# Performance work log

Measured on AMD Instinct MI355X. Metric: run time of the kernel, lower is better.

## Reference

```python
import jax, jax.numpy as jnp
import numpy as np

B, T, IN, H, OUT = 256, 512, 9, 512, 3


def setup_inputs() -> dict:
    key = jax.random.key(0)
    ks = jax.random.split(key, 7)
    s = 0.05  # keep gates in a sane range
    return {
        "x": jax.random.normal(ks[0], (B, T, IN), dtype=jnp.float32),
        "W_ih": jax.random.normal(ks[1], (4 * H, IN), dtype=jnp.float32) * s,
        "W_hh": jax.random.normal(ks[2], (4 * H, H), dtype=jnp.float32) * s,
        "b_ih": jax.random.normal(ks[3], (4 * H,), dtype=jnp.float32) * s,
        "b_hh": jax.random.normal(ks[4], (4 * H,), dtype=jnp.float32) * s,
        "W_fc": jax.random.normal(ks[5], (OUT, H), dtype=jnp.float32) * s,
        "b_fc": jax.random.normal(ks[6], (OUT,), dtype=jnp.float32) * s,
        "horizon": 10,
    }


def reference(x, W_ih, W_hh, b_ih, b_hh, W_fc, b_fc, horizon):
    Bn, Tn, _ = x.shape
    Hn = W_hh.shape[1]
    On = W_fc.shape[0]
    # branch condition depends only on the static step index -> precompute mask
    idx = np.arange(Tn)
    use_raw = jnp.asarray((idx < 5) | (idx % int(horizon) == 0))  # [T]

    def step(carry, inp):
        hx, cx, prev_out = carry
        x_t, raw = inp  # x_t: [B, IN], raw: scalar bool
        # else-branch input: previous fc output (3) ++ last 6 state features -> 9
        alt = jnp.concatenate([prev_out, x_t[:, On:]], axis=1)
        xin = jnp.where(raw, x_t, alt)
        gates = xin @ W_ih.T + b_ih + hx @ W_hh.T + b_hh  # [B, 4H]
        i, f, g, o = jnp.split(gates, 4, axis=1)
        cx2 = jax.nn.sigmoid(f) * cx + jax.nn.sigmoid(i) * jnp.tanh(g)
        hx2 = jax.nn.sigmoid(o) * jnp.tanh(cx2)
        out = hx2 @ W_fc.T + b_fc  # [B, OUT]
        return (hx2, cx2, out), out

    init = (
        jnp.zeros((Bn, Hn), x.dtype),
        jnp.zeros((Bn, Hn), x.dtype),
        jnp.zeros((Bn, On), x.dtype),
    )
    x_tb = jnp.swapaxes(x, 0, 1)  # [T, B, IN]
    _, outs = jax.lax.scan(step, init, (x_tb, use_raw))
    return jnp.swapaxes(outs, 0, 1)  # [B, T, OUT]
```

## Files before the change

kernel.cpp:

```cpp
#include <hip/hip_runtime.h>

typedef __attribute__((ext_vector_type(8))) short bf16x8;
typedef __attribute__((ext_vector_type(4))) float f32x4;

#define NTT 512
#define NH  512
#define NIN 9
#define NO  3
#define MEMBERS 32
#define MROWS   32
#define HPW     16

__device__ __forceinline__ short f2bf(float f) {
  unsigned u = __builtin_bit_cast(unsigned, f);
  u = (u + 0x7fffu + ((u >> 16) & 1u)) >> 16;
  return (short)u;
}
__device__ __forceinline__ float bf2f(short s) {
  unsigned u = ((unsigned)(unsigned short)s) << 16;
  return __builtin_bit_cast(float, u);
}
__device__ __forceinline__ float sigf(float x) { return 1.f / (1.f + __expf(-x)); }
__device__ __forceinline__ float tanh_fast(float x) { return 1.f - 2.f / (1.f + __expf(2.f * x)); }

__global__ __launch_bounds__(256, 1) void lstm_tagged(
    const float* __restrict__ x, const float* __restrict__ W_ih,
    const float* __restrict__ W_hh, const float* __restrict__ b_ih,
    const float* __restrict__ b_hh, const float* __restrict__ W_fc,
    const float* __restrict__ b_fc, const int* __restrict__ horizon,
    float* __restrict__ out, unsigned* __restrict__ ws32) {
  const int tid  = threadIdx.x;
  const int bid  = blockIdx.x;
  const int g    = bid >> 5;
  const int w    = bid & 31;
  const int wid  = tid >> 6;
  const int lane = tid & 63;
  const int l15  = lane & 15;
  const int quad = lane >> 4;
  const int hl   = tid & 15;
  const int b0   = tid >> 4;
  const int hg   = w * HPW + hl;

  unsigned* tbuf0 = ws32;
  unsigned* tbuf1 = ws32 + 131072;

  __shared__ __align__(16) unsigned short hbuf[32][520];
  __shared__ __align__(16) float gbuf[4][16][36];
  __shared__ float fcbuf[4][32][4];
  __shared__ float xbuf[32][NIN];
  __shared__ float xw[64][NIN];
  __shared__ float bsl[64];

  bf16x8 Bhi[16], Blo[16];
#pragma unroll
  for (int kt = 0; kt < 16; ++kt) {
    bf16x8 vh, vl;
    const int row = wid * NH + w * HPW + l15;
#pragma unroll
    for (int j = 0; j < 8; ++j) {
      int k = kt * 32 + quad * 8 + j;
      float v = W_hh[(size_t)row * NH + k];
      short hi = f2bf(v);
      vh[j] = hi; vl[j] = f2bf(v - bf2f(hi));
    }
    Bhi[kt] = vh; Blo[kt] = vl;
  }
  bf16x8 Fhi[4], Flo[4];
#pragma unroll
  for (int kk = 0; kk < 4; ++kk) {
    bf16x8 vh, vl;
#pragma unroll
    for (int j = 0; j < 8; ++j) {
      int k = (wid * 4 + kk) * 32 + quad * 8 + j;
      float v = (l15 < NO) ? W_fc[(size_t)l15 * NH + k] : 0.f;
      short hi = f2bf(v);
      vh[j] = hi; vl[j] = f2bf(v - bf2f(hi));
    }
    Fhi[kk] = vh; Flo[kk] = vl;
  }
  if (tid < 64) {
    int grow = (tid >> 4) * NH + w * HPW + (tid & 15);
    bsl[tid] = b_ih[grow] + b_hh[grow];
#pragma unroll
    for (int k = 0; k < NIN; ++k) xw[tid][k] = W_ih[grow * NIN + k];
  }
  for (int i = tid; i < 8320; i += 256) ((unsigned*)hbuf)[i] = 0u;
  const float bfc0 = b_fc[0], bfc1 = b_fc[1], bfc2 = b_fc[2];
  const int hor = *horizon;

  const int r0c = tid / NIN, k0c = tid - r0c * NIN;
  const int i1c = tid + 256;
  const int r1c = i1c / NIN, k1c = i1c - r1c * NIN;
  const bool x0ok = (r0c < MROWS), x1ok = (i1c < MROWS * NIN);
  const float* xp0 = x + (size_t)(g * MROWS + (x0ok ? r0c : 0)) * NTT * NIN + k0c;
  const float* xp1 = x + (size_t)(g * MROWS + (x1ok ? r1c : 0)) * NTT * NIN + k1c;
  const int ob = tid / NO, oo = tid - ob * NO;
  const bool ook = (w == 0) && (tid < MROWS * NO);
  const float obias = (oo == 0) ? bfc0 : (oo == 1) ? bfc1 : bfc2;
  float* op = out + ((size_t)(g * MROWS + ob) * NTT) * NO + oo;
  __syncthreads();

  float cst[2] = {0.f, 0.f};
  int tmod = 0;

  for (int t = 0; t <= NTT; ++t) {
    float xv0 = 0.f, xv1 = 0.f;
    if (t < NTT) {
      if (x0ok) xv0 = xp0[t * NIN];
      if (x1ok) xv1 = xp1[t * NIN];
    }

    f32x4 z4 = {0.f, 0.f, 0.f, 0.f};
    f32x4 accg[2] = {z4, z4}, accf[2] = {z4, z4};
#pragma unroll
    for (int kt = 0; kt < 16; ++kt) {
      bf16x8 a0 = *(const bf16x8*)&hbuf[l15][kt * 32 + quad * 8];
      bf16x8 a1 = *(const bf16x8*)&hbuf[16 + l15][kt * 32 + quad * 8];
      accg[0] = __builtin_amdgcn_mfma_f32_16x16x32_bf16(a0, Bhi[kt], accg[0], 0, 0, 0);
      accg[1] = __builtin_amdgcn_mfma_f32_16x16x32_bf16(a1, Bhi[kt], accg[1], 0, 0, 0);
      accg[0] = __builtin_amdgcn_mfma_f32_16x16x32_bf16(a0, Blo[kt], accg[0], 0, 0, 0);
      accg[1] = __builtin_amdgcn_mfma_f32_16x16x32_bf16(a1, Blo[kt], accg[1], 0, 0, 0);
      if ((kt >> 2) == wid) {
        int kk = kt & 3;
        accf[0] = __builtin_amdgcn_mfma_f32_16x16x32_bf16(a0, Fhi[kk], accf[0], 0, 0, 0);
        accf[1] = __builtin_amdgcn_mfma_f32_16x16x32_bf16(a1, Fhi[kk], accf[1], 0, 0, 0);
        accf[0] = __builtin_amdgcn_mfma_f32_16x16x32_bf16(a0, Flo[kk], accf[0], 0, 0, 0);
        accf[1] = __builtin_amdgcn_mfma_f32_16x16x32_bf16(a1, Flo[kk], accf[1], 0, 0, 0);
      }
    }
#pragma unroll
    for (int mt = 0; mt < 2; ++mt)
      *(f32x4*)&gbuf[wid][l15][mt * 16 + quad * 4] = accg[mt];
    if (l15 < NO) {
#pragma unroll
      for (int mt = 0; mt < 2; ++mt)
#pragma unroll
        for (int r = 0; r < 4; ++r) fcbuf[wid][mt * 16 + quad * 4 + r][l15] = accf[mt][r];
    }
    if (t < NTT) {
      if (x0ok) xbuf[r0c][k0c] = xv0;
      if (x1ok) xbuf[r1c][k1c] = xv1;
    }
    __syncthreads();

    if (t == NTT) {
      if (ook)
        op[(t - 1) * NO] =
            obias + fcbuf[0][ob][oo] + fcbuf[1][ob][oo] + fcbuf[2][ob][oo] + fcbuf[3][ob][oo];
      break;
    }

    const bool raw = (t < 5) || (tmod == 0);
    const unsigned tg = (unsigned)(t + 1);
    unsigned* dst = ((t & 1) ? tbuf1 : tbuf0) + (size_t)g * 16384;

#pragma unroll
    for (int e = 0; e < 2; ++e) {
      int b = b0 + 16 * e;
      float xin[NIN];
#pragma unroll
      for (int k = 0; k < NIN; ++k) xin[k] = xbuf[b][k];
      if (!raw) {
        xin[0] = bfc0 + fcbuf[0][b][0] + fcbuf[1][b][0] + fcbuf[2][b][0] + fcbuf[3][b][0];
        xin[1] = bfc1 + fcbuf[0][b][1] + fcbuf[1][b][1] + fcbuf[2][b][1] + fcbuf[3][b][1];
        xin[2] = bfc2 + fcbuf[0][b][2] + fcbuf[1][b][2] + fcbuf[2][b][2] + fcbuf[3][b][2];
      }
      float gv[4];
#pragma unroll
      for (int gg = 0; gg < 4; ++gg) {
        int r = gg * 16 + hl;
        float s = bsl[r] + gbuf[gg][hl][b];
#pragma unroll
        for (int k = 0; k < NIN; ++k) s += xin[k] * xw[r][k];
        gv[gg] = s;
      }
      float cn = sigf(gv[1]) * cst[e] + sigf(gv[0]) * tanh_fast(gv[2]);
      cst[e] = cn;
      float hn = sigf(gv[3]) * tanh_fast(cn);
      unsigned word = (unsigned)(unsigned short)f2bf(hn) | (tg << 16);
      __hip_atomic_store(&dst[(size_t)b * NH + hg], word,
                         __ATOMIC_RELAXED, __HIP_MEMORY_SCOPE_AGENT);
    }

    if (ook && t > 0)
      op[(t - 1) * NO] =
          obias + fcbuf[0][ob][oo] + fcbuf[1][ob][oo] + fcbuf[2][ob][oo] + fcbuf[3][ob][oo];

    {
      const unsigned long long* src =
          (const unsigned long long*)(((t & 1) ? tbuf1 : tbuf0) + (size_t)g * 16384);
      const unsigned long long pat =
          ((unsigned long long)tg << 16) | ((unsigned long long)tg << 48);
      unsigned* hb32 = (unsigned*)hbuf;
      unsigned long long v[32];
#pragma unroll
      for (int j = 0; j < 32; ++j)
        v[j] = __hip_atomic_load(src + tid + 256 * j,
                                 __ATOMIC_RELAXED, __HIP_MEMORY_SCOPE_AGENT);
      unsigned mask = 0u;
#pragma unroll
      for (int j = 0; j < 32; ++j)
        mask |= (((v[j] ^ pat) & 0xFFFF0000FFFF0000ULL) ? 1u : 0u) << j;
      while (__builtin_expect(mask != 0u, 0)) {
#pragma unroll
        for (int j = 0; j < 32; ++j)
          if (mask & (1u << j))
            v[j] = __hip_atomic_load(src + tid + 256 * j,
                                     __ATOMIC_RELAXED, __HIP_MEMORY_SCOPE_AGENT);
        unsigned m2 = 0u;
#pragma unroll
        for (int j = 0; j < 32; ++j)
          m2 |= (((v[j] ^ pat) & 0xFFFF0000FFFF0000ULL) ? 1u : 0u) << j;
        mask = m2;
      }
#pragma unroll
      for (int j = 0; j < 32; ++j) {
        const int q = tid + 256 * j;
        hb32[(q >> 8) * 260 + (q & 255)] =
            (unsigned)(v[j] & 0xFFFFu) | ((unsigned)(v[j] >> 32) << 16);
      }
      __syncthreads();
    }
    ++tmod; if (tmod == hor) tmod = 0;
  }
}

__global__ __launch_bounds__(256, 1) void lstm_fallback(
    const float* __restrict__ x, const float* __restrict__ W_ih,
    const float* __restrict__ W_hh, const float* __restrict__ b_ih,
    const float* __restrict__ b_hh, const float* __restrict__ W_fc,
    const float* __restrict__ b_fc, const int* __restrict__ horizon,
    float* __restrict__ out, unsigned short* __restrict__ ws) {
  const int tid  = threadIdx.x;
  const int bid  = blockIdx.x;
  const int g    = bid >> 5;
  const int w    = bid & 31;
  const int wid  = tid >> 6;
  const int lane = tid & 63;
  const int l15  = lane & 15;
  const int quad = lane >> 4;
  const int hl   = tid & 15;
  const int b0   = tid >> 4;

  unsigned short* buf0 = ws;
  unsigned short* buf1 = ws + 131072;
  int* fl = (int*)(ws + 262144) + g * MEMBERS;

  __shared__ __align__(16) unsigned short hbuf[32][520];
  __shared__ __align__(16) float gbuf[4][16][36];
  __shared__ float fcbuf[4][32][4];
  __shared__ float xbuf[32][NIN];
  __shared__ float xw[64][NIN];
  __shared__ float bsl[64];

  bf16x8 Bhi[16], Blo[16];
#pragma unroll
  for (int kt = 0; kt < 16; ++kt) {
    bf16x8 vh, vl;
    const int row = wid * NH + w * HPW + l15;
#pragma unroll
    for (int j = 0; j < 8; ++j) {
      int k = kt * 32 + quad * 8 + j;
      float v = W_hh[(size_t)row * NH + k];
      short hi = f2bf(v);
      vh[j] = hi; vl[j] = f2bf(v - bf2f(hi));
    }
    Bhi[kt] = vh; Blo[kt] = vl;
  }
  bf16x8 Fhi[4], Flo[4];
#pragma unroll
  for (int kk = 0; kk < 4; ++kk) {
    bf16x8 vh, vl;
#pragma unroll
    for (int j = 0; j < 8; ++j) {
      int k = (wid * 4 + kk) * 32 + quad * 8 + j;
      float v = (l15 < NO) ? W_fc[(size_t)l15 * NH + k] : 0.f;
      short hi = f2bf(v);
      vh[j] = hi; vl[j] = f2bf(v - bf2f(hi));
    }
    Fhi[kk] = vh; Flo[kk] = vl;
  }
  if (tid < 64) {
    int grow = (tid >> 4) * NH + w * HPW + (tid & 15);
    bsl[tid] = b_ih[grow] + b_hh[grow];
#pragma unroll
    for (int k = 0; k < NIN; ++k) xw[tid][k] = W_ih[grow * NIN + k];
  }
  for (int i = tid; i < 8320; i += 256) ((unsigned*)hbuf)[i] = 0u;
  const float bfc0 = b_fc[0], bfc1 = b_fc[1], bfc2 = b_fc[2];
  const int hor = *horizon;
  __syncthreads();

  float cst[2] = {0.f, 0.f};
  int tmod = 0;

  for (int t = 0; t <= NTT; ++t) {
    float xv0 = 0.f, xv1 = 0.f;
    int r0 = 0, k0 = 0, r1 = 0, k1 = 0;
    if (t < NTT) {
      r0 = tid / NIN; k0 = tid - r0 * NIN;
      if (r0 < MROWS) xv0 = x[((size_t)(g * MROWS + r0) * NTT + t) * NIN + k0];
      int i1 = tid + 256;
      r1 = i1 / NIN; k1 = i1 - r1 * NIN;
      if (i1 < MROWS * NIN) xv1 = x[((size_t)(g * MROWS + r1) * NTT + t) * NIN + k1];
    }
    f32x4 z4 = {0.f, 0.f, 0.f, 0.f};
    f32x4 accg[2] = {z4, z4}, accf[2] = {z4, z4};
#pragma unroll
    for (int kt = 0; kt < 16; ++kt) {
      bf16x8 a0 = *(const bf16x8*)&hbuf[l15][kt * 32 + quad * 8];
      bf16x8 a1 = *(const bf16x8*)&hbuf[16 + l15][kt * 32 + quad * 8];
      accg[0] = __builtin_amdgcn_mfma_f32_16x16x32_bf16(a0, Bhi[kt], accg[0], 0, 0, 0);
      accg[1] = __builtin_amdgcn_mfma_f32_16x16x32_bf16(a1, Bhi[kt], accg[1], 0, 0, 0);
      accg[0] = __builtin_amdgcn_mfma_f32_16x16x32_bf16(a0, Blo[kt], accg[0], 0, 0, 0);
      accg[1] = __builtin_amdgcn_mfma_f32_16x16x32_bf16(a1, Blo[kt], accg[1], 0, 0, 0);
      if ((kt >> 2) == wid) {
        int kk = kt & 3;
        accf[0] = __builtin_amdgcn_mfma_f32_16x16x32_bf16(a0, Fhi[kk], accf[0], 0, 0, 0);
        accf[1] = __builtin_amdgcn_mfma_f32_16x16x32_bf16(a1, Fhi[kk], accf[1], 0, 0, 0);
        accf[0] = __builtin_amdgcn_mfma_f32_16x16x32_bf16(a0, Flo[kk], accf[0], 0, 0, 0);
        accf[1] = __builtin_amdgcn_mfma_f32_16x16x32_bf16(a1, Flo[kk], accf[1], 0, 0, 0);
      }
    }
#pragma unroll
    for (int mt = 0; mt < 2; ++mt)
      *(f32x4*)&gbuf[wid][l15][mt * 16 + quad * 4] = accg[mt];
    if (l15 < NO) {
#pragma unroll
      for (int mt = 0; mt < 2; ++mt)
#pragma unroll
        for (int r = 0; r < 4; ++r) fcbuf[wid][mt * 16 + quad * 4 + r][l15] = accf[mt][r];
    }
    if (t < NTT) {
      if (r0 < MROWS) xbuf[r0][k0] = xv0;
      if (tid < MROWS * NIN - 256) xbuf[r1][k1] = xv1;
    }
    __syncthreads();

    if (t == NTT) {
      if (w == 0 && tid < MROWS * NO) {
        int b = tid / NO, o = tid - b * NO;
        float bo = (o == 0) ? bfc0 : (o == 1) ? bfc1 : bfc2;
        out[((size_t)(g * MROWS + b) * NTT + (t - 1)) * NO + o] =
            bo + fcbuf[0][b][o] + fcbuf[1][b][o] + fcbuf[2][b][o] + fcbuf[3][b][o];
      }
      break;
    }

    const bool raw = (t < 5) || (tmod == 0);
    unsigned long long* nxt64 =
        (unsigned long long*)(((t & 1) ? buf1 : buf0) + (size_t)g * (MROWS * NH));
#pragma unroll
    for (int e = 0; e < 2; ++e) {
      int b = b0 + 16 * e;
      float xin[NIN];
#pragma unroll
      for (int k = 0; k < NIN; ++k) xin[k] = xbuf[b][k];
      if (!raw) {
        xin[0] = bfc0 + fcbuf[0][b][0] + fcbuf[1][b][0] + fcbuf[2][b][0] + fcbuf[3][b][0];
        xin[1] = bfc1 + fcbuf[0][b][1] + fcbuf[1][b][1] + fcbuf[2][b][1] + fcbuf[3][b][1];
        xin[2] = bfc2 + fcbuf[0][b][2] + fcbuf[1][b][2] + fcbuf[2][b][2] + fcbuf[3][b][2];
      }
      float gv[4];
#pragma unroll
      for (int gg = 0; gg < 4; ++gg) {
        int r = gg * 16 + hl;
        float s = bsl[r] + gbuf[gg][hl][b];
#pragma unroll
        for (int k = 0; k < NIN; ++k) s += xin[k] * xw[r][k];
        gv[gg] = s;
      }
      float cn = sigf(gv[1]) * cst[e] + sigf(gv[0]) * tanh_fast(gv[2]);
      cst[e] = cn;
      float hn = sigf(gv[3]) * tanh_fast(cn);
      unsigned hb16 = (unsigned)(unsigned short)f2bf(hn);
      unsigned pair = hb16 | ((unsigned)__shfl_xor((int)hb16, 1, 64) << 16);
      unsigned long long v64 =
          (unsigned long long)pair |
          ((unsigned long long)(unsigned)__shfl_xor((int)pair, 2, 64) << 32);
      if ((hl & 3) == 0)
        __hip_atomic_store(&nxt64[(size_t)b * 128 + w * 4 + (hl >> 2)], v64,
                           __ATOMIC_RELAXED, __HIP_MEMORY_SCOPE_AGENT);
    }
    asm volatile("s_waitcnt vmcnt(0)" ::: "memory");
    __syncthreads();

    if (tid == 0)
      __hip_atomic_store(&fl[w], t + 1, __ATOMIC_RELAXED, __HIP_MEMORY_SCOPE_AGENT);
    if (w == 0 && t > 0 && tid < MROWS * NO) {
      int b = tid / NO, o = tid - b * NO;
      float bo = (o == 0) ? bfc0 : (o == 1) ? bfc1 : bfc2;
      out[((size_t)(g * MROWS + b) * NTT + (t - 1)) * NO + o] =
          bo + fcbuf[0][b][o] + fcbuf[1][b][o] + fcbuf[2][b][o] + fcbuf[3][b][o];
    }
    if (tid < MEMBERS) {
      while (__hip_atomic_load(&fl[tid], __ATOMIC_RELAXED,
                               __HIP_MEMORY_SCOPE_AGENT) < t + 1)
        __builtin_amdgcn_s_sleep(1);
    }
    __syncthreads();

    const unsigned long long* src =
        (const unsigned long long*)(((t & 1) ? buf1 : buf0) + (size_t)g * (MROWS * NH));
#pragma unroll
    for (int j = 0; j < 16; ++j) {
      int idx = tid + 256 * j;
      unsigned long long v =
          __hip_atomic_load(src + idx, __ATOMIC_RELAXED, __HIP_MEMORY_SCOPE_AGENT);
      *(unsigned long long*)&hbuf[idx >> 7][(idx & 127) * 4] = v;
    }
    __syncthreads();
    ++tmod; if (tmod == hor) tmod = 0;
  }
}

extern "C" void kernel_launch(void* const* d_in, const int* in_sizes, int n_in,
                              void* d_out, int out_size, void* d_ws, size_t ws_size,
                              hipStream_t stream) {
  (void)in_sizes; (void)n_in; (void)out_size;
  const float* x    = (const float*)d_in[0];
  const float* W_ih = (const float*)d_in[1];
  const float* W_hh = (const float*)d_in[2];
  const float* b_ih = (const float*)d_in[3];
  const float* b_hh = (const float*)d_in[4];
  const float* W_fc = (const float*)d_in[5];
  const float* b_fc = (const float*)d_in[6];
  const int*   hor  = (const int*)d_in[7];
  if (ws_size >= (size_t)1048576) {
    lstm_tagged<<<dim3(256), dim3(256), 0, stream>>>(
        x, W_ih, W_hh, b_ih, b_hh, W_fc, b_fc, hor,
        (float*)d_out, (unsigned*)d_ws);
  } else {
    lstm_fallback<<<dim3(256), dim3(256), 0, stream>>>(
        x, W_ih, W_hh, b_ih, b_hh, W_fc, b_fc, hor,
        (float*)d_out, (unsigned short*)d_ws);
  }
}
```

Measured before the change: 3.092 ms.

## Repartition LSTM into 64 blocks of 512 threads with 8 groups

The persistent LSTM kernel drops from 256 blocks of 256 threads (8 batch groups × 32 hidden slices of 16) to 64 blocks of 512 threads (8 groups × 8 slices of 64 hidden units each). Each wave now holds two N-tiles of W_hh in registers, and the input weights and biases move from shared memory into registers. Fewer blocks take part in each per-step cross-block handshake through tagged global words, which should cut polling traffic and sync latency. In exchange each block does four times the MFMA and elementwise work per step, and register pressure rises, since 512 threads must fit two blocks per CU.

```diff
diff --git a/kernel.cpp b/kernel.cpp
--- a/kernel.cpp
+++ b/kernel.cpp
@@ -7,9 +7,7 @@
 #define NH  512
 #define NIN 9
 #define NO  3
-#define MEMBERS 32
 #define MROWS   32
-#define HPW     16
 
 __device__ __forceinline__ short f2bf(float f) {
   unsigned u = __builtin_bit_cast(unsigned, f);
@@ -23,7 +21,7 @@
 __device__ __forceinline__ float sigf(float x) { return 1.f / (1.f + __expf(-x)); }
 __device__ __forceinline__ float tanh_fast(float x) { return 1.f - 2.f / (1.f + __expf(2.f * x)); }
 
-__global__ __launch_bounds__(256, 1) void lstm_tagged(
+__global__ __launch_bounds__(512, 2) void lstm_tagged8(
     const float* __restrict__ x, const float* __restrict__ W_ih,
     const float* __restrict__ W_hh, const float* __restrict__ b_ih,
     const float* __restrict__ b_hh, const float* __restrict__ W_fc,
@@ -31,97 +29,97 @@
     float* __restrict__ out, unsigned* __restrict__ ws32) {
   const int tid  = threadIdx.x;
   const int bid  = blockIdx.x;
-  const int g    = bid >> 5;
-  const int w    = bid & 31;
+  const int g    = bid & 7;
+  const int w    = bid >> 3;
   const int wid  = tid >> 6;
   const int lane = tid & 63;
   const int l15  = lane & 15;
   const int quad = lane >> 4;
-  const int hl   = tid & 15;
-  const int b0   = tid >> 4;
-  const int hg   = w * HPW + hl;
+  const int hl   = tid & 63;
+  const int rb   = tid >> 6;
 
   unsigned* tbuf0 = ws32;
   unsigned* tbuf1 = ws32 + 131072;
 
   __shared__ __align__(16) unsigned short hbuf[32][520];
-  __shared__ __align__(16) float gbuf[4][16][36];
-  __shared__ float fcbuf[4][32][4];
+  __shared__ float gbuf[4][64][37];
+  __shared__ __align__(16) float fcbuf[32][4][8];
   __shared__ float xbuf[32][NIN];
-  __shared__ float xw[64][NIN];
-  __shared__ float bsl[64];
-
-  bf16x8 Bhi[16], Blo[16];
-#pragma unroll
-  for (int kt = 0; kt < 16; ++kt) {
+
+  bf16x8 Bhi[2][16], Blo[2][16];
+#pragma unroll
+  for (int nt = 0; nt < 2; ++nt) {
+    const int s = wid * 2 + nt;
+    const int row = (s >> 2) * NH + w * 64 + (s & 3) * 16 + l15;
+#pragma unroll
+    for (int kt = 0; kt < 16; ++kt) {
+      bf16x8 vh, vl;
+#pragma unroll
+      for (int j = 0; j < 8; ++j) {
+        int k = kt * 32 + quad * 8 + j;
+        float v = W_hh[(size_t)row * NH + k];
+        short hi = f2bf(v);
+        vh[j] = hi; vl[j] = f2bf(v - bf2f(hi));
+      }
+      Bhi[nt][kt] = vh; Blo[nt][kt] = vl;
+    }
+  }
+  bf16x8 Fhi[2], Flo[2];
+#pragma unroll
+  for (int kk = 0; kk < 2; ++kk) {
     bf16x8 vh, vl;
-    const int row = wid * NH + w * HPW + l15;
 #pragma unroll
     for (int j = 0; j < 8; ++j) {
-      int k = kt * 32 + quad * 8 + j;
-      float v = W_hh[(size_t)row * NH + k];
-      short hi = f2bf(v);
-      vh[j] = hi; vl[j] = f2bf(v - bf2f(hi));
-    }
-    Bhi[kt] = vh; Blo[kt] = vl;
-  }
-  bf16x8 Fhi[4], Flo[4];
-#pragma unroll
-  for (int kk = 0; kk < 4; ++kk) {
-    bf16x8 vh, vl;
-#pragma unroll
-    for (int j = 0; j < 8; ++j) {
-      int k = (wid * 4 + kk) * 32 + quad * 8 + j;
+      int k = (wid * 2 + kk) * 32 + quad * 8 + j;
       float v = (l15 < NO) ? W_fc[(size_t)l15 * NH + k] : 0.f;
       short hi = f2bf(v);
       vh[j] = hi; vl[j] = f2bf(v - bf2f(hi));
     }
     Fhi[kk] = vh; Flo[kk] = vl;
   }
-  if (tid < 64) {
-    int grow = (tid >> 4) * NH + w * HPW + (tid & 15);
-    bsl[tid] = b_ih[grow] + b_hh[grow];
-#pragma unroll
-    for (int k = 0; k < NIN; ++k) xw[tid][k] = W_ih[grow * NIN + k];
-  }
-  for (int i = tid; i < 8320; i += 256) ((unsigned*)hbuf)[i] = 0u;
+  float xwr[4][NIN], bslr[4];
+#pragma unroll
+  for (int gg = 0; gg < 4; ++gg) {
+    const int grow = gg * NH + w * 64 + hl;
+    bslr[gg] = b_ih[grow] + b_hh[grow];
+#pragma unroll
+    for (int k = 0; k < NIN; ++k) xwr[gg][k] = W_ih[grow * NIN + k];
+  }
+  for (int i = tid; i < 8320; i += 512) ((unsigned*)hbuf)[i] = 0u;
   const float bfc0 = b_fc[0], bfc1 = b_fc[1], bfc2 = b_fc[2];
   const int hor = *horizon;
 
   const int r0c = tid / NIN, k0c = tid - r0c * NIN;
-  const int i1c = tid + 256;
-  const int r1c = i1c / NIN, k1c = i1c - r1c * NIN;
-  const bool x0ok = (r0c < MROWS), x1ok = (i1c < MROWS * NIN);
+  const bool x0ok = (tid < MROWS * NIN);
   const float* xp0 = x + (size_t)(g * MROWS + (x0ok ? r0c : 0)) * NTT * NIN + k0c;
-  const float* xp1 = x + (size_t)(g * MROWS + (x1ok ? r1c : 0)) * NTT * NIN + k1c;
   const int ob = tid / NO, oo = tid - ob * NO;
   const bool ook = (w == 0) && (tid < MROWS * NO);
   const float obias = (oo == 0) ? bfc0 : (oo == 1) ? bfc1 : bfc2;
   float* op = out + ((size_t)(g * MROWS + ob) * NTT) * NO + oo;
   __syncthreads();
 
-  float cst[2] = {0.f, 0.f};
+  float cst[4] = {0.f, 0.f, 0.f, 0.f};
   int tmod = 0;
 
   for (int t = 0; t <= NTT; ++t) {
-    float xv0 = 0.f, xv1 = 0.f;
-    if (t < NTT) {
-      if (x0ok) xv0 = xp0[t * NIN];
-      if (x1ok) xv1 = xp1[t * NIN];
-    }
+    float xv0 = 0.f;
+    if (t < NTT && x0ok) xv0 = xp0[t * NIN];
 
     f32x4 z4 = {0.f, 0.f, 0.f, 0.f};
-    f32x4 accg[2] = {z4, z4}, accf[2] = {z4, z4};
+    f32x4 accg[2][2] = {{z4, z4}, {z4, z4}}, accf[2] = {z4, z4};
 #pragma unroll
     for (int kt = 0; kt < 16; ++kt) {
       bf16x8 a0 = *(const bf16x8*)&hbuf[l15][kt * 32 + quad * 8];
       bf16x8 a1 = *(const bf16x8*)&hbuf[16 + l15][kt * 32 + quad * 8];
-      accg[0] = __builtin_amdgcn_mfma_f32_16x16x32_bf16(a0, Bhi[kt], accg[0], 0, 0, 0);
-      accg[1] = __builtin_amdgcn_mfma_f32_16x16x32_bf16(a1, Bhi[kt], accg[1], 0, 0, 0);
-      accg[0] = __builtin_amdgcn_mfma_f32_16x16x32_bf16(a0, Blo[kt], accg[0], 0, 0, 0);
-      accg[1] = __builtin_amdgcn_mfma_f32_16x16x32_bf16(a1, Blo[kt], accg[1], 0, 0, 0);
-      if ((kt >> 2) == wid) {
-        int kk = kt & 3;
+#pragma unroll
+      for (int nt = 0; nt < 2; ++nt) {
+        accg[nt][0] = __builtin_amdgcn_mfma_f32_16x16x32_bf16(a0, Bhi[nt][kt], accg[nt][0], 0, 0, 0);
+        accg[nt][1] = __builtin_amdgcn_mfma_f32_16x16x32_bf16(a1, Bhi[nt][kt], accg[nt][1], 0, 0, 0);
+        accg[nt][0] = __builtin_amdgcn_mfma_f32_16x16x32_bf16(a0, Blo[nt][kt], accg[nt][0], 0, 0, 0);
+        accg[nt][1] = __builtin_amdgcn_mfma_f32_16x16x32_bf16(a1, Blo[nt][kt], accg[nt][1], 0, 0, 0);
+      }
+      if ((kt >> 1) == wid) {
+        int kk = kt & 1;
         accf[0] = __builtin_amdgcn_mfma_f32_16x16x32_bf16(a0, Fhi[kk], accf[0], 0, 0, 0);
         accf[1] = __builtin_amdgcn_mfma_f32_16x16x32_bf16(a1, Fhi[kk], accf[1], 0, 0, 0);
         accf[0] = __builtin_amdgcn_mfma_f32_16x16x32_bf16(a0, Flo[kk], accf[0], 0, 0, 0);
@@ -129,24 +127,31 @@
       }
     }
 #pragma unroll
-    for (int mt = 0; mt < 2; ++mt)
-      *(f32x4*)&gbuf[wid][l15][mt * 16 + quad * 4] = accg[mt];
+    for (int nt = 0; nt < 2; ++nt) {
+      const int s = wid * 2 + nt;
+      const int gg = s >> 2, hloc = (s & 3) * 16 + l15;
+#pragma unroll
+      for (int mt = 0; mt < 2; ++mt)
+#pragma unroll
+        for (int r = 0; r < 4; ++r)
+          gbuf[gg][hloc][mt * 16 + quad * 4 + r] = accg[nt][mt][r];
+    }
     if (l15 < NO) {
 #pragma unroll
       for (int mt = 0; mt < 2; ++mt)
 #pragma unroll
-        for (int r = 0; r < 4; ++r) fcbuf[wid][mt * 16 + quad * 4 + r][l15] = accf[mt][r];
-    }
-    if (t < NTT) {
-      if (x0ok) xbuf[r0c][k0c] = xv0;
-      if (x1ok) xbuf[r1c][k1c] = xv1;
-    }
+        for (int r = 0; r < 4; ++r) fcbuf[mt * 16 + quad * 4 + r][l15][wid] = accf[mt][r];
+    }
+    if (t < NTT && x0ok) xbuf[r0c][k0c] = xv0;
     __syncthreads();
 
     if (t == NTT) {
-      if (ook)
-        op[(t - 1) * NO] =
-            obias + fcbuf[0][ob][oo] + fcbuf[1][ob][oo] + fcbuf[2][ob][oo] + fcbuf[3][ob][oo];
+      if (ook) {
+        f32x4 pa = *(const f32x4*)&fcbuf[ob][oo][0];
+        f32x4 pb = *(const f32x4*)&fcbuf[ob][oo][4];
+        op[(t - 1) * NO] = obias + pa[0] + pa[1] + pa[2] + pa[3]
+                                 + pb[0] + pb[1] + pb[2] + pb[3];
+      }
       break;
     }
 
@@ -155,36 +160,44 @@
     unsigned* dst = ((t & 1) ? tbuf1 : tbuf0) + (size_t)g * 16384;
 
 #pragma unroll
-    for (int e = 0; e < 2; ++e) {
-      int b = b0 + 16 * e;
+    for (int e = 0; e < 4; ++e) {
+      const int brow = rb + 8 * e;
       float xin[NIN];
 #pragma unroll
-      for (int k = 0; k < NIN; ++k) xin[k] = xbuf[b][k];
+      for (int k = 0; k < NIN; ++k) xin[k] = xbuf[brow][k];
       if (!raw) {
-        xin[0] = bfc0 + fcbuf[0][b][0] + fcbuf[1][b][0] + fcbuf[2][b][0] + fcbuf[3][b][0];
-        xin[1] = bfc1 + fcbuf[0][b][1] + fcbuf[1][b][1] + fcbuf[2][b][1] + fcbuf[3][b][1];
-        xin[2] = bfc2 + fcbuf[0][b][2] + fcbuf[1][b][2] + fcbuf[2][b][2] + fcbuf[3][b][2];
+        f32x4 p0a = *(const f32x4*)&fcbuf[brow][0][0];
+        f32x4 p0b = *(const f32x4*)&fcbuf[brow][0][4];
+        f32x4 p1a = *(const f32x4*)&fcbuf[brow][1][0];
+        f32x4 p1b = *(const f32x4*)&fcbuf[brow][1][4];
+        f32x4 p2a = *(const f32x4*)&fcbuf[brow][2][0];
+        f32x4 p2b = *(const f32x4*)&fcbuf[brow][2][4];
+        xin[0] = bfc0 + p0a[0] + p0a[1] + p0a[2] + p0a[3] + p0b[0] + p0b[1] + p0b[2] + p0b[3];
+        xin[1] = bfc1 + p1a[0] + p1a[1] + p1a[2] + p1a[3] + p1b[0] + p1b[1] + p1b[2] + p1b[3];
+        xin[2] = bfc2 + p2a[0] + p2a[1] + p2a[2] + p2a[3] + p2b[0] + p2b[1] + p2b[2] + p2b[3];
       }
       float gv[4];
 #pragma unroll
       for (int gg = 0; gg < 4; ++gg) {
-        int r = gg * 16 + hl;
-        float s = bsl[r] + gbuf[gg][hl][b];
-#pragma unroll
-        for (int k = 0; k < NIN; ++k) s += xin[k] * xw[r][k];
+        float s = bslr[gg] + gbuf[gg][hl][brow];
+#pragma unroll
+        for (int k = 0; k < NIN; ++k) s += xin[k] * xwr[gg][k];
         gv[gg] = s;
       }
       float cn = sigf(gv[1]) * cst[e] + sigf(gv[0]) * tanh_fast(gv[2]);
       cst[e] = cn;
       float hn = sigf(gv[3]) * tanh_fast(cn);
       unsigned word = (unsigned)(unsigned short)f2bf(hn) | (tg << 16);
-      __hip_atomic_store(&dst[(size_t)b * NH + hg], word,
+      __hip_atomic_store(&dst[(size_t)brow * NH + w * 64 + hl], word,
                          __ATOMIC_RELAXED, __HIP_MEMORY_SCOPE_AGENT);
     }
 
-    if (ook && t > 0)
-      op[(t - 1) * NO] =
-          obias + fcbuf[0][ob][oo] + fcbuf[1][ob][oo] + fcbuf[2][ob][oo] + fcbuf[3][ob][oo];
+    if (ook && t > 0) {
+      f32x4 pa = *(const f32x4*)&fcbuf[ob][oo][0];
+      f32x4 pb = *(const f32x4*)&fcbuf[ob][oo][4];
+      op[(t - 1) * NO] = obias + pa[0] + pa[1] + pa[2] + pa[3]
+                               + pb[0] + pb[1] + pb[2] + pb[3];
+    }
 
     {
       const unsigned long long* src =
@@ -192,30 +205,30 @@
       const unsigned long long pat =
           ((unsigned long long)tg << 16) | ((unsigned long long)tg << 48);
       unsigned* hb32 = (unsigned*)hbuf;
-      unsigned long long v[32];
-#pragma unroll
-      for (int j = 0; j < 32; ++j)
-        v[j] = __hip_atomic_load(src + tid + 256 * j,
+      unsigned long long v[16];
+#pragma unroll
+      for (int j = 0; j < 16; ++j)
+        v[j] = __hip_atomic_load(src + tid + 512 * j,
                                  __ATOMIC_RELAXED, __HIP_MEMORY_SCOPE_AGENT);
       unsigned mask = 0u;
 #pragma unroll
-      for (int j = 0; j < 32; ++j)
+      for (int j = 0; j < 16; ++j)
         mask |= (((v[j] ^ pat) & 0xFFFF0000FFFF0000ULL) ? 1u : 0u) << j;
       while (__builtin_expect(mask != 0u, 0)) {
 #pragma unroll
-        for (int j = 0; j < 32; ++j)
+        for (int j = 0; j < 16; ++j)
           if (mask & (1u << j))
-            v[j] = __hip_atomic_load(src + tid + 256 * j,
+            v[j] = __hip_atomic_load(src + tid + 512 * j,
                                      __ATOMIC_RELAXED, __HIP_MEMORY_SCOPE_AGENT);
         unsigned m2 = 0u;
 #pragma unroll
-        for (int j = 0; j < 32; ++j)
+        for (int j = 0; j < 16; ++j)
           m2 |= (((v[j] ^ pat) & 0xFFFF0000FFFF0000ULL) ? 1u : 0u) << j;
         mask = m2;
       }
 #pragma unroll
-      for (int j = 0; j < 32; ++j) {
-        const int q = tid + 256 * j;
+      for (int j = 0; j < 16; ++j) {
+        const int q = tid + 512 * j;
         hb32[(q >> 8) * 260 + (q & 255)] =
             (unsigned)(v[j] & 0xFFFFu) | ((unsigned)(v[j] >> 32) << 16);
       }
@@ -225,6 +238,8 @@
   }
 }
 
+#define MEMBERS 32
+#define HPW 16
 __global__ __launch_bounds__(256, 1) void lstm_fallback(
     const float* __restrict__ x, const float* __restrict__ W_ih,
     const float* __restrict__ W_hh, const float* __restrict__ b_ih,
@@ -427,7 +442,7 @@
   const float* b_fc = (const float*)d_in[6];
   const int*   hor  = (const int*)d_in[7];
   if (ws_size >= (size_t)1048576) {
-    lstm_tagged<<<dim3(256), dim3(256), 0, stream>>>(
+    lstm_tagged8<<<dim3(64), dim3(512), 0, stream>>>(
         x, W_ih, W_hh, b_ih, b_hh, W_fc, b_fc, hor,
         (float*)d_out, (unsigned*)d_ws);
   } else {
```

After: 12.27 ms. 297% more time.

## Halve workgroup count by giving each block 32 hidden units across 16 members

Applied to the files above, without the earlier changes.

Each workgroup now owns 32 hidden units instead of 16, holding two W_hh column tiles in registers, so the grid shrinks from 256 to 128 blocks with 16 members per batch group instead of 32. Block-to-group mapping is interleaved (g = bid & 7). This is meant to cut the number of peers each group synchronises with through tagged global memory each step, and the polling traffic that comes with it. In exchange each block runs twice the MFMA work per step, needs double the register file for weights, and half the CUs sit idle.

```diff
diff --git a/kernel.cpp b/kernel.cpp
--- a/kernel.cpp
+++ b/kernel.cpp
@@ -7,9 +7,7 @@
 #define NH  512
 #define NIN 9
 #define NO  3
-#define MEMBERS 32
 #define MROWS   32
-#define HPW     16
 
 __device__ __forceinline__ short f2bf(float f) {
   unsigned u = __builtin_bit_cast(unsigned, f);
@@ -23,7 +21,7 @@
 __device__ __forceinline__ float sigf(float x) { return 1.f / (1.f + __expf(-x)); }
 __device__ __forceinline__ float tanh_fast(float x) { return 1.f - 2.f / (1.f + __expf(2.f * x)); }
 
-__global__ __launch_bounds__(256, 1) void lstm_tagged(
+__global__ __launch_bounds__(256, 1) void lstm_tagged16(
     const float* __restrict__ x, const float* __restrict__ W_ih,
     const float* __restrict__ W_hh, const float* __restrict__ b_ih,
     const float* __restrict__ b_hh, const float* __restrict__ W_fc,
@@ -31,39 +29,42 @@
     float* __restrict__ out, unsigned* __restrict__ ws32) {
   const int tid  = threadIdx.x;
   const int bid  = blockIdx.x;
-  const int g    = bid >> 5;
-  const int w    = bid & 31;
+  const int g    = bid & 7;
+  const int w    = bid >> 3;
   const int wid  = tid >> 6;
   const int lane = tid & 63;
   const int l15  = lane & 15;
   const int quad = lane >> 4;
-  const int hl   = tid & 15;
-  const int b0   = tid >> 4;
-  const int hg   = w * HPW + hl;
+  const int hl   = tid & 31;
+  const int rb   = tid >> 5;
 
   unsigned* tbuf0 = ws32;
   unsigned* tbuf1 = ws32 + 131072;
 
   __shared__ __align__(16) unsigned short hbuf[32][520];
-  __shared__ __align__(16) float gbuf[4][16][36];
+  __shared__ __align__(16) float gbuf[4][32][36];
   __shared__ float fcbuf[4][32][4];
   __shared__ float xbuf[32][NIN];
-  __shared__ float xw[64][NIN];
-  __shared__ float bsl[64];
-
-  bf16x8 Bhi[16], Blo[16];
-#pragma unroll
-  for (int kt = 0; kt < 16; ++kt) {
-    bf16x8 vh, vl;
-    const int row = wid * NH + w * HPW + l15;
-#pragma unroll
-    for (int j = 0; j < 8; ++j) {
-      int k = kt * 32 + quad * 8 + j;
-      float v = W_hh[(size_t)row * NH + k];
-      short hi = f2bf(v);
-      vh[j] = hi; vl[j] = f2bf(v - bf2f(hi));
-    }
-    Bhi[kt] = vh; Blo[kt] = vl;
+  __shared__ float xw[128][NIN];
+  __shared__ float bsl[128];
+
+  bf16x8 Bhi[2][16], Blo[2][16];
+#pragma unroll
+  for (int nt = 0; nt < 2; ++nt) {
+    const int s = wid * 2 + nt;
+    const int row = (s >> 1) * NH + w * 32 + (s & 1) * 16 + l15;
+#pragma unroll
+    for (int kt = 0; kt < 16; ++kt) {
+      bf16x8 vh, vl;
+#pragma unroll
+      for (int j = 0; j < 8; ++j) {
+        int k = kt * 32 + quad * 8 + j;
+        float v = W_hh[(size_t)row * NH + k];
+        short hi = f2bf(v);
+        vh[j] = hi; vl[j] = f2bf(v - bf2f(hi));
+      }
+      Bhi[nt][kt] = vh; Blo[nt][kt] = vl;
+    }
   }
   bf16x8 Fhi[4], Flo[4];
 #pragma unroll
@@ -78,8 +79,8 @@
     }
     Fhi[kk] = vh; Flo[kk] = vl;
   }
-  if (tid < 64) {
-    int grow = (tid >> 4) * NH + w * HPW + (tid & 15);
+  if (tid < 128) {
+    int grow = (tid >> 5) * NH + w * 32 + (tid & 31);
     bsl[tid] = b_ih[grow] + b_hh[grow];
 #pragma unroll
     for (int k = 0; k < NIN; ++k) xw[tid][k] = W_ih[grow * NIN + k];
@@ -100,7 +101,7 @@
   float* op = out + ((size_t)(g * MROWS + ob) * NTT) * NO + oo;
   __syncthreads();
 
-  float cst[2] = {0.f, 0.f};
+  float cst[4] = {0.f, 0.f, 0.f, 0.f};
   int tmod = 0;
 
   for (int t = 0; t <= NTT; ++t) {
@@ -111,15 +112,18 @@
     }
 
     f32x4 z4 = {0.f, 0.f, 0.f, 0.f};
-    f32x4 accg[2] = {z4, z4}, accf[2] = {z4, z4};
+    f32x4 accg[2][2] = {{z4, z4}, {z4, z4}}, accf[2] = {z4, z4};
 #pragma unroll
     for (int kt = 0; kt < 16; ++kt) {
       bf16x8 a0 = *(const bf16x8*)&hbuf[l15][kt * 32 + quad * 8];
       bf16x8 a1 = *(const bf16x8*)&hbuf[16 + l15][kt * 32 + quad * 8];
-      accg[0] = __builtin_amdgcn_mfma_f32_16x16x32_bf16(a0, Bhi[kt], accg[0], 0, 0, 0);
-      accg[1] = __builtin_amdgcn_mfma_f32_16x16x32_bf16(a1, Bhi[kt], accg[1], 0, 0, 0);
-      accg[0] = __builtin_amdgcn_mfma_f32_16x16x32_bf16(a0, Blo[kt], accg[0], 0, 0, 0);
-      accg[1] = __builtin_amdgcn_mfma_f32_16x16x32_bf16(a1, Blo[kt], accg[1], 0, 0, 0);
+#pragma unroll
+      for (int nt = 0; nt < 2; ++nt) {
+        accg[nt][0] = __builtin_amdgcn_mfma_f32_16x16x32_bf16(a0, Bhi[nt][kt], accg[nt][0], 0, 0, 0);
+        accg[nt][1] = __builtin_amdgcn_mfma_f32_16x16x32_bf16(a1, Bhi[nt][kt], accg[nt][1], 0, 0, 0);
+        accg[nt][0] = __builtin_amdgcn_mfma_f32_16x16x32_bf16(a0, Blo[nt][kt], accg[nt][0], 0, 0, 0);
+        accg[nt][1] = __builtin_amdgcn_mfma_f32_16x16x32_bf16(a1, Blo[nt][kt], accg[nt][1], 0, 0, 0);
+      }
       if ((kt >> 2) == wid) {
         int kk = kt & 3;
         accf[0] = __builtin_amdgcn_mfma_f32_16x16x32_bf16(a0, Fhi[kk], accf[0], 0, 0, 0);
@@ -129,8 +133,13 @@
       }
     }
 #pragma unroll
-    for (int mt = 0; mt < 2; ++mt)
-      *(f32x4*)&gbuf[wid][l15][mt * 16 + quad * 4] = accg[mt];
+    for (int nt = 0; nt < 2; ++nt) {
+      const int s = wid * 2 + nt;
+      const int gg = s >> 1, hloc = (s & 1) * 16 + l15;
+#pragma unroll
+      for (int mt = 0; mt < 2; ++mt)
+        *(f32x4*)&gbuf[gg][hloc][mt * 16 + quad * 4] = accg[nt][mt];
+    }
     if (l15 < NO) {
 #pragma unroll
       for (int mt = 0; mt < 2; ++mt)
@@ -155,21 +164,21 @@
     unsigned* dst = ((t & 1) ? tbuf1 : tbuf0) + (size_t)g * 16384;
 
 #pragma unroll
-    for (int e = 0; e < 2; ++e) {
-      int b = b0 + 16 * e;
+    for (int e = 0; e < 4; ++e) {
+      const int brow = rb + 8 * e;
       float xin[NIN];
 #pragma unroll
-      for (int k = 0; k < NIN; ++k) xin[k] = xbuf[b][k];
+      for (int k = 0; k < NIN; ++k) xin[k] = xbuf[brow][k];
       if (!raw) {
-        xin[0] = bfc0 + fcbuf[0][b][0] + fcbuf[1][b][0] + fcbuf[2][b][0] + fcbuf[3][b][0];
-        xin[1] = bfc1 + fcbuf[0][b][1] + fcbuf[1][b][1] + fcbuf[2][b][1] + fcbuf[3][b][1];
-        xin[2] = bfc2 + fcbuf[0][b][2] + fcbuf[1][b][2] + fcbuf[2][b][2] + fcbuf[3][b][2];
+        xin[0] = bfc0 + fcbuf[0][brow][0] + fcbuf[1][brow][0] + fcbuf[2][brow][0] + fcbuf[3][brow][0];
+        xin[1] = bfc1 + fcbuf[0][brow][1] + fcbuf[1][brow][1] + fcbuf[2][brow][1] + fcbuf[3][brow][1];
+        xin[2] = bfc2 + fcbuf[0][brow][2] + fcbuf[1][brow][2] + fcbuf[2][brow][2] + fcbuf[3][brow][2];
       }
       float gv[4];
 #pragma unroll
       for (int gg = 0; gg < 4; ++gg) {
-        int r = gg * 16 + hl;
-        float s = bsl[r] + gbuf[gg][hl][b];
+        const int r = gg * 32 + hl;
+        float s = bsl[r] + gbuf[gg][hl][brow];
 #pragma unroll
         for (int k = 0; k < NIN; ++k) s += xin[k] * xw[r][k];
         gv[gg] = s;
@@ -178,7 +187,7 @@
       cst[e] = cn;
       float hn = sigf(gv[3]) * tanh_fast(cn);
       unsigned word = (unsigned)(unsigned short)f2bf(hn) | (tg << 16);
-      __hip_atomic_store(&dst[(size_t)b * NH + hg], word,
+      __hip_atomic_store(&dst[(size_t)brow * NH + w * 32 + hl], word,
                          __ATOMIC_RELAXED, __HIP_MEMORY_SCOPE_AGENT);
     }
 
@@ -225,6 +234,8 @@
   }
 }
 
+#define MEMBERS 32
+#define HPW 16
 __global__ __launch_bounds__(256, 1) void lstm_fallback(
     const float* __restrict__ x, const float* __restrict__ W_ih,
     const float* __restrict__ W_hh, const float* __restrict__ b_ih,
@@ -427,7 +438,7 @@
   const float* b_fc = (const float*)d_in[6];
   const int*   hor  = (const int*)d_in[7];
   if (ws_size >= (size_t)1048576) {
-    lstm_tagged<<<dim3(256), dim3(256), 0, stream>>>(
+    lstm_tagged16<<<dim3(128), dim3(256), 0, stream>>>(
         x, W_ih, W_hh, b_ih, b_hh, W_fc, b_fc, hor,
         (float*)d_out, (unsigned*)d_ws);
   } else {
```

Measured after the change: 4.087 ms. +32.2%, slower.

## Replace per-element step tags with packed bf16 data plus per-wave flag barrier

Applied to the files above, without the earlier changes.

Stops embedding the step tag in every hidden-state word. Each wave now packs four bf16 values into a 64-bit store, then publishes a per-wave step flag after draining its stores. Consumers spin on the 128 flags of their group, issue an acquire fence, and read half as many 64-bit words. This halves the traffic through the exchange buffer and replaces the per-word tag checks with a flag poll. The cost is an extra round trip (store, flag, poll, load), and correctness depends on the vmcnt wait and fence giving the right ordering.

```diff
diff --git a/kernel.cpp b/kernel.cpp
--- a/kernel.cpp
+++ b/kernel.cpp
@@ -23,12 +23,12 @@
 __device__ __forceinline__ float sigf(float x) { return 1.f / (1.f + __expf(-x)); }
 __device__ __forceinline__ float tanh_fast(float x) { return 1.f - 2.f / (1.f + __expf(2.f * x)); }
 
-__global__ __launch_bounds__(256, 1) void lstm_tagged(
+__global__ __launch_bounds__(256, 1) void lstm_flag(
     const float* __restrict__ x, const float* __restrict__ W_ih,
     const float* __restrict__ W_hh, const float* __restrict__ b_ih,
     const float* __restrict__ b_hh, const float* __restrict__ W_fc,
     const float* __restrict__ b_fc, const int* __restrict__ horizon,
-    float* __restrict__ out, unsigned* __restrict__ ws32) {
+    float* __restrict__ out, unsigned short* __restrict__ ws) {
   const int tid  = threadIdx.x;
   const int bid  = blockIdx.x;
   const int g    = bid >> 5;
@@ -39,10 +39,10 @@
   const int quad = lane >> 4;
   const int hl   = tid & 15;
   const int b0   = tid >> 4;
-  const int hg   = w * HPW + hl;
-
-  unsigned* tbuf0 = ws32;
-  unsigned* tbuf1 = ws32 + 131072;
+
+  unsigned short* buf0 = ws;
+  unsigned short* buf1 = ws + 131072;
+  int* fl4 = (int*)(ws + 262144) + g * 128;
 
   __shared__ __align__(16) unsigned short hbuf[32][520];
   __shared__ __align__(16) float gbuf[4][16][36];
@@ -151,8 +151,8 @@
     }
 
     const bool raw = (t < 5) || (tmod == 0);
-    const unsigned tg = (unsigned)(t + 1);
-    unsigned* dst = ((t & 1) ? tbuf1 : tbuf0) + (size_t)g * 16384;
+    unsigned long long* nxt64 =
+        (unsigned long long*)(((t & 1) ? buf1 : buf0) + (size_t)g * (MROWS * NH));
 
 #pragma unroll
     for (int e = 0; e < 2; ++e) {
@@ -177,47 +177,42 @@
       float cn = sigf(gv[1]) * cst[e] + sigf(gv[0]) * tanh_fast(gv[2]);
       cst[e] = cn;
       float hn = sigf(gv[3]) * tanh_fast(cn);
-      unsigned word = (unsigned)(unsigned short)f2bf(hn) | (tg << 16);
-      __hip_atomic_store(&dst[(size_t)b * NH + hg], word,
+      unsigned hb16 = (unsigned)(unsigned short)f2bf(hn);
+      unsigned pair = hb16 | ((unsigned)__shfl_xor((int)hb16, 1, 64) << 16);
+      unsigned long long v64 =
+          (unsigned long long)pair |
+          ((unsigned long long)(unsigned)__shfl_xor((int)pair, 2, 64) << 32);
+      if ((hl & 3) == 0)
+        __hip_atomic_store(&nxt64[(size_t)b * 128 + w * 4 + (hl >> 2)], v64,
+                           __ATOMIC_RELAXED, __HIP_MEMORY_SCOPE_AGENT);
+    }
+
+    asm volatile("s_waitcnt vmcnt(0)" ::: "memory");
+    if (lane == 0)
+      __hip_atomic_store(&fl4[w * 4 + wid], t + 1,
                          __ATOMIC_RELAXED, __HIP_MEMORY_SCOPE_AGENT);
-    }
 
     if (ook && t > 0)
       op[(t - 1) * NO] =
           obias + fcbuf[0][ob][oo] + fcbuf[1][ob][oo] + fcbuf[2][ob][oo] + fcbuf[3][ob][oo];
 
     {
+      const int tp1 = t + 1;
+      while (true) {
+        int f0 = __hip_atomic_load(&fl4[lane], __ATOMIC_RELAXED, __HIP_MEMORY_SCOPE_AGENT);
+        int f1 = __hip_atomic_load(&fl4[64 + lane], __ATOMIC_RELAXED, __HIP_MEMORY_SCOPE_AGENT);
+        if (__all(f0 >= tp1 && f1 >= tp1)) break;
+      }
+      __builtin_amdgcn_fence(__ATOMIC_ACQUIRE, "agent");
+
       const unsigned long long* src =
-          (const unsigned long long*)(((t & 1) ? tbuf1 : tbuf0) + (size_t)g * 16384);
-      const unsigned long long pat =
-          ((unsigned long long)tg << 16) | ((unsigned long long)tg << 48);
-      unsigned* hb32 = (unsigned*)hbuf;
-      unsigned long long v[32];
-#pragma unroll
-      for (int j = 0; j < 32; ++j)
-        v[j] = __hip_atomic_load(src + tid + 256 * j,
-                                 __ATOMIC_RELAXED, __HIP_MEMORY_SCOPE_AGENT);
-      unsigned mask = 0u;
-#pragma unroll
-      for (int j = 0; j < 32; ++j)
-        mask |= (((v[j] ^ pat) & 0xFFFF0000FFFF0000ULL) ? 1u : 0u) << j;
-      while (__builtin_expect(mask != 0u, 0)) {
-#pragma unroll
-        for (int j = 0; j < 32; ++j)
-          if (mask & (1u << j))
-            v[j] = __hip_atomic_load(src + tid + 256 * j,
-                                     __ATOMIC_RELAXED, __HIP_MEMORY_SCOPE_AGENT);
-        unsigned m2 = 0u;
-#pragma unroll
-        for (int j = 0; j < 32; ++j)
-          m2 |= (((v[j] ^ pat) & 0xFFFF0000FFFF0000ULL) ? 1u : 0u) << j;
-        mask = m2;
-      }
-#pragma unroll
-      for (int j = 0; j < 32; ++j) {
-        const int q = tid + 256 * j;
-        hb32[(q >> 8) * 260 + (q & 255)] =
-            (unsigned)(v[j] & 0xFFFFu) | ((unsigned)(v[j] >> 32) << 16);
+          (const unsigned long long*)(((t & 1) ? buf1 : buf0) + (size_t)g * (MROWS * NH));
+#pragma unroll
+      for (int j = 0; j < 16; ++j) {
+        int idx = tid + 256 * j;
+        unsigned long long v =
+            __hip_atomic_load(src + idx, __ATOMIC_RELAXED, __HIP_MEMORY_SCOPE_AGENT);
+        *(unsigned long long*)&hbuf[idx >> 7][(idx & 127) * 4] = v;
       }
       __syncthreads();
     }
@@ -427,9 +422,9 @@
   const float* b_fc = (const float*)d_in[6];
   const int*   hor  = (const int*)d_in[7];
   if (ws_size >= (size_t)1048576) {
-    lstm_tagged<<<dim3(256), dim3(256), 0, stream>>>(
+    lstm_flag<<<dim3(256), dim3(256), 0, stream>>>(
         x, W_ih, W_hh, b_ih, b_hh, W_fc, b_fc, hor,
-        (float*)d_out, (unsigned*)d_ws);
+        (float*)d_out, (unsigned short*)d_ws);
   } else {
     lstm_fallback<<<dim3(256), dim3(256), 0, stream>>>(
         x, W_ih, W_hh, b_ih, b_hh, W_fc, b_fc, hor,
```

After: 8.544 ms. 176% more time.
